# Kernel tuning notes

Measured on AMD Instinct MI355X. Metric: run time of the kernel, lower is better.

## Reference

```python
import jax, jax.numpy as jnp
import numpy as np

N, IN_DIM, OUT_DIM, HEADS = 3072, 512, 64, 8
EDGE_PROB = 0.01
NEG_SLOPE = 0.2


def setup_inputs() -> dict:
    key = jax.random.key(0)
    k1, k2, k3, k4, k5 = jax.random.split(key, 5)
    x = jax.random.normal(k1, (N, IN_DIM), dtype=jnp.float32)
    # sparse-ish dense adjacency mask with self-loops
    adj = (jax.random.uniform(k2, (N, N)) < EDGE_PROB).astype(jnp.float32)
    adj = jnp.maximum(adj, jnp.eye(N, dtype=jnp.float32))
    W = jax.random.normal(k3, (HEADS, IN_DIM, OUT_DIM), dtype=jnp.float32) * 0.1
    a_src = jax.random.normal(k4, (HEADS, OUT_DIM), dtype=jnp.float32) * 0.1
    a_dst = jax.random.normal(k5, (HEADS, OUT_DIM), dtype=jnp.float32) * 0.1
    return {"x": x, "adj": adj, "W": W, "a_src": a_src, "a_dst": a_dst}


def reference(x, adj, W, a_src, a_dst):
    # per-head linear projection: [H, N, OUT]
    h = jnp.einsum("ni,hio->hno", x, W)
    # attention logits e_ij = LeakyReLU(a_src . h_i + a_dst . h_j)
    f_src = jnp.einsum("hno,ho->hn", h, a_src)  # [H, N]
    f_dst = jnp.einsum("hno,ho->hn", h, a_dst)  # [H, N]
    e = f_src[:, :, None] + f_dst[:, None, :]   # [H, N, N]
    e = jax.nn.leaky_relu(e, negative_slope=NEG_SLOPE)
    # mask non-edges, row-softmax over neighbors
    e = jnp.where(adj[None] > 0, e, jnp.float32(-1e9))
    att = jax.nn.softmax(e, axis=-1)             # [H, N, N]
    # aggregate neighbor features per head
    out = jnp.einsum("hij,hjo->hio", att, h)     # [H, N, OUT]
    # concat heads along feature dim -> [N, H*OUT]
    return out.transpose(1, 0, 2).reshape(N, HEADS * OUT_DIM)
```

## Files before the change

### kernel.cpp

```cpp
#include <hip/hip_runtime.h>

#define N_NODES 3072
#define IN_DIM 512
#define OUT_DIM 64
#define HEADS 8
#define NEG_SLOPE 0.2f
#define MAX_E 128

typedef __attribute__((ext_vector_type(8))) short bf16x8;
typedef __attribute__((ext_vector_type(4))) float f32x4;

#define XFRAG_TILES (N_NODES / 16)
#define KTILES (IN_DIM / 32)
#define XFRAG_THREADS (XFRAG_TILES * KTILES * 64)
#define WFRAG_THREADS (HEADS * KTILES * 4 * 64)

__device__ inline unsigned short f2bf(float f) {
    union { float f; unsigned u; } v; v.f = f;
    unsigned r = (v.u + 0x7FFF + ((v.u >> 16) & 1)) >> 16;
    return (unsigned short)r;
}

__global__ __launch_bounds__(256) void gat_prep(
    const float* __restrict__ x, const float* __restrict__ W,
    short* __restrict__ xfrag, short* __restrict__ wfrag) {
    int tid = blockIdx.x * 256 + threadIdx.x;
    if (tid < XFRAG_THREADS) {
        int lane = tid & 63;
        int kt = (tid >> 6) & (KTILES - 1);
        int rt = tid >> 10;
        int m = rt * 16 + (lane & 15);
        int k0 = kt * 32 + (lane >> 4) * 8;
        const float4* xp = (const float4*)(x + (size_t)m * IN_DIM + k0);
        float4 v0 = xp[0], v1 = xp[1];
        bf16x8 r;
        r[0] = (short)f2bf(v0.x); r[1] = (short)f2bf(v0.y);
        r[2] = (short)f2bf(v0.z); r[3] = (short)f2bf(v0.w);
        r[4] = (short)f2bf(v1.x); r[5] = (short)f2bf(v1.y);
        r[6] = (short)f2bf(v1.z); r[7] = (short)f2bf(v1.w);
        ((bf16x8*)xfrag)[tid] = r;
    } else {
        int t2 = tid - XFRAG_THREADS;
        if (t2 >= WFRAG_THREADS) return;
        int lane = t2 & 63;
        int c = (t2 >> 6) & 3;
        int kt = (t2 >> 8) & (KTILES - 1);
        int head = t2 >> 12;
        int n = c * 16 + (lane & 15);
        int k0 = kt * 32 + (lane >> 4) * 8;
        const float* wp = W + ((size_t)head * IN_DIM + k0) * OUT_DIM + n;
        bf16x8 r;
#pragma unroll
        for (int j = 0; j < 8; ++j) r[j] = (short)f2bf(wp[(size_t)j * OUT_DIM]);
        ((bf16x8*)wfrag)[t2] = r;
    }
}

__global__ __launch_bounds__(256) void gat_proj(
    const short* __restrict__ xfrag, const short* __restrict__ wfrag,
    const float* __restrict__ a_src, const float* __restrict__ a_dst,
    unsigned short* __restrict__ hb, float* __restrict__ fsrc, float* __restrict__ fdst) {
    __shared__ float hs[32][OUT_DIM + 1];

    const int t = threadIdx.x;
    const int lane = t & 63;
    const int w = t >> 6;
    const int head = blockIdx.y;
    const int m0 = blockIdx.x * 32;
    const int rt0 = blockIdx.x * 2;

    const bf16x8* xa = (const bf16x8*)xfrag + (size_t)rt0 * 16 * 64 + lane;
    const bf16x8* wb = (const bf16x8*)wfrag + ((size_t)head * KTILES * 4 + w) * 64 + lane;

    f32x4 acc0 = {0.f, 0.f, 0.f, 0.f};
    f32x4 acc1 = {0.f, 0.f, 0.f, 0.f};
#pragma unroll
    for (int kt = 0; kt < KTILES; ++kt) {
        bf16x8 a0 = xa[kt * 64];
        bf16x8 a1 = xa[(16 + kt) * 64];
        bf16x8 b  = wb[kt * 4 * 64];
        acc0 = __builtin_amdgcn_mfma_f32_16x16x32_bf16(a0, b, acc0, 0, 0, 0);
        acc1 = __builtin_amdgcn_mfma_f32_16x16x32_bf16(a1, b, acc1, 0, 0, 0);
    }

    const int col = w * 16 + (lane & 15);
    const int r0 = (lane >> 4) * 4;
    unsigned short* hp = hb + (size_t)m0 * (HEADS * OUT_DIM) + head * OUT_DIM + col;
#pragma unroll
    for (int i2 = 0; i2 < 4; ++i2) {
        hs[r0 + i2][col] = acc0[i2];
        hs[r0 + 16 + i2][col] = acc1[i2];
        hp[(size_t)(r0 + i2) * (HEADS * OUT_DIM)] = f2bf(acc0[i2]);
        hp[(size_t)(r0 + 16 + i2) * (HEADS * OUT_DIM)] = f2bf(acc1[i2]);
    }
    __syncthreads();

    {
        const float* av = (t < 128 ? a_src : a_dst) + head * OUT_DIM;
        const int tt = t & 127;
        const int row = tt >> 2, part = tt & 3;
        float s = 0.f;
#pragma unroll
        for (int n = 0; n < 16; ++n) s += hs[row][part * 16 + n] * av[part * 16 + n];
        s += __shfl_xor(s, 1, 64);
        s += __shfl_xor(s, 2, 64);
        if (part == 0) {
            float* dst = (t < 128 ? fsrc : fdst);
            dst[head * N_NODES + m0 + row] = s;
        }
    }
}

__global__ __launch_bounds__(256) void gat_agg(
    const float* __restrict__ adj, const unsigned short* __restrict__ hb,
    const float* __restrict__ fsrc, const float* __restrict__ fdst,
    float* __restrict__ out) {
    __shared__ int s_idx[MAX_E];
    __shared__ float s_p[HEADS][MAX_E];
    __shared__ int s_cnt;

    const int i = blockIdx.x;
    const int t = threadIdx.x;
    if (t == 0) s_cnt = 0;
    __syncthreads();

    const float4* arow4 = (const float4*)(adj + (size_t)i * N_NODES);
#pragma unroll
    for (int it = 0; it < 3; ++it) {
        const int jj = t + it * 256;
        float4 v = arow4[jj];
        const int j = jj * 4;
        if (v.x > 0.f) { int s = atomicAdd(&s_cnt, 1); if (s < MAX_E) s_idx[s] = j; }
        if (v.y > 0.f) { int s = atomicAdd(&s_cnt, 1); if (s < MAX_E) s_idx[s] = j + 1; }
        if (v.z > 0.f) { int s = atomicAdd(&s_cnt, 1); if (s < MAX_E) s_idx[s] = j + 2; }
        if (v.w > 0.f) { int s = atomicAdd(&s_cnt, 1); if (s < MAX_E) s_idx[s] = j + 3; }
    }
    __syncthreads();
    const int E = min(s_cnt, MAX_E);

    const int w = t >> 6;
    const int lane = t & 63;
    const int half = lane >> 5;
    const int sl = lane & 31;
    const int head = 2 * w + half;

    const float fi = fsrc[head * N_NODES + i];

    float m = -1e30f;
    for (int k = sl; k < E; k += 32) {
        float e = fi + fdst[head * N_NODES + s_idx[k]];
        e = e > 0.f ? e : NEG_SLOPE * e;
        s_p[head][k] = e;
        m = fmaxf(m, e);
    }
#pragma unroll
    for (int o = 16; o; o >>= 1) m = fmaxf(m, __shfl_xor(m, o, 64));

    float sum = 0.f;
    for (int k = sl; k < E; k += 32) {
        float p = __expf(s_p[head][k] - m);
        s_p[head][k] = p;
        sum += p;
    }
#pragma unroll
    for (int o = 16; o; o >>= 1) sum += __shfl_xor(sum, o, 64);
    const float inv = 1.f / sum;

    __syncthreads();

    const unsigned short* hbase = hb + head * OUT_DIM + sl * 2;
    float a0 = 0.f, a1 = 0.f;
#pragma unroll 8
    for (int k = 0; k < E; ++k) {
        const int j = s_idx[k];
        const float p = s_p[head][k];
        const unsigned u = *(const unsigned*)(hbase + (size_t)j * (HEADS * OUT_DIM));
        a0 = fmaf(p, __uint_as_float(u << 16), a0);
        a1 = fmaf(p, __uint_as_float(u & 0xffff0000u), a1);
    }
    float2 r = {a0 * inv, a1 * inv};
    *(float2*)(out + (size_t)i * (HEADS * OUT_DIM) + head * OUT_DIM + sl * 2) = r;
}

extern "C" void kernel_launch(void* const* d_in, const int* in_sizes, int n_in,
                              void* d_out, int out_size, void* d_ws, size_t ws_size,
                              hipStream_t stream) {
    const float* x     = (const float*)d_in[0];
    const float* adj   = (const float*)d_in[1];
    const float* W     = (const float*)d_in[2];
    const float* a_src = (const float*)d_in[3];
    const float* a_dst = (const float*)d_in[4];
    float* out = (float*)d_out;

    float* fsrc = (float*)d_ws;
    float* fdst = fsrc + HEADS * N_NODES;
    unsigned short* hb = (unsigned short*)(fdst + HEADS * N_NODES);
    short* xfrag = (short*)(hb + (size_t)N_NODES * HEADS * OUT_DIM);
    short* wfrag = xfrag + (size_t)XFRAG_TILES * KTILES * 64 * 8;

    gat_prep<<<(XFRAG_THREADS + WFRAG_THREADS) / 256, 256, 0, stream>>>(
        x, W, xfrag, wfrag);
    gat_proj<<<dim3(N_NODES / 32, HEADS), 256, 0, stream>>>(
        xfrag, wfrag, a_src, a_dst, hb, fsrc, fdst);
    gat_agg<<<N_NODES, 256, 0, stream>>>(adj, hb, fsrc, fdst, out);
}
```

Before: 108.2 us.

## Move adjacency scan into prep kernel so it overlaps bf16 conversion

The adjacency-row scan that builds each node's neighbor list moves out of the aggregation kernel and into the prep kernel, which now runs extra blocks alongside the x/W bf16 fragment conversion. Neighbor indices and counts go to workspace, and the aggregation kernel reads them instead of streaming the 36 MB dense adjacency matrix. The aim is to run the bandwidth-heavy adjacency read in parallel with independent prep work and to shorten the critical aggregation kernel. It costs an extra global write and read of the compact edge lists, plus more workspace.

```diff
diff --git a/kernel.cpp b/kernel.cpp
--- a/kernel.cpp
+++ b/kernel.cpp
@@ -14,6 +14,7 @@
 #define KTILES (IN_DIM / 32)
 #define XFRAG_THREADS (XFRAG_TILES * KTILES * 64)
 #define WFRAG_THREADS (HEADS * KTILES * 4 * 64)
+#define PREP_BLOCKS ((XFRAG_THREADS + WFRAG_THREADS) / 256)
 
 __device__ inline unsigned short f2bf(float f) {
     union { float f; unsigned u; } v; v.f = f;
@@ -21,38 +22,69 @@
     return (unsigned short)r;
 }
 
-__global__ __launch_bounds__(256) void gat_prep(
+__global__ __launch_bounds__(256) void gat_prep_scan(
     const float* __restrict__ x, const float* __restrict__ W,
-    short* __restrict__ xfrag, short* __restrict__ wfrag) {
-    int tid = blockIdx.x * 256 + threadIdx.x;
-    if (tid < XFRAG_THREADS) {
-        int lane = tid & 63;
-        int kt = (tid >> 6) & (KTILES - 1);
-        int rt = tid >> 10;
-        int m = rt * 16 + (lane & 15);
-        int k0 = kt * 32 + (lane >> 4) * 8;
-        const float4* xp = (const float4*)(x + (size_t)m * IN_DIM + k0);
-        float4 v0 = xp[0], v1 = xp[1];
-        bf16x8 r;
-        r[0] = (short)f2bf(v0.x); r[1] = (short)f2bf(v0.y);
-        r[2] = (short)f2bf(v0.z); r[3] = (short)f2bf(v0.w);
-        r[4] = (short)f2bf(v1.x); r[5] = (short)f2bf(v1.y);
-        r[6] = (short)f2bf(v1.z); r[7] = (short)f2bf(v1.w);
-        ((bf16x8*)xfrag)[tid] = r;
+    const float* __restrict__ adj,
+    short* __restrict__ xfrag, short* __restrict__ wfrag,
+    int* __restrict__ e_idx, int* __restrict__ e_cnt) {
+    __shared__ int s_idx[MAX_E];
+    __shared__ int s_cnt;
+
+    const int b = blockIdx.x;
+    const int t = threadIdx.x;
+
+    if (b < N_NODES) {
+        const int i = b;
+        if (t == 0) s_cnt = 0;
+        __syncthreads();
+
+        const float4* arow4 = (const float4*)(adj + (size_t)i * N_NODES);
+#pragma unroll
+        for (int it = 0; it < 3; ++it) {
+            const int jj = t + it * 256;
+            float4 v = arow4[jj];
+            const int j = jj * 4;
+            if (v.x > 0.f) { int s = atomicAdd(&s_cnt, 1); if (s < MAX_E) s_idx[s] = j; }
+            if (v.y > 0.f) { int s = atomicAdd(&s_cnt, 1); if (s < MAX_E) s_idx[s] = j + 1; }
+            if (v.z > 0.f) { int s = atomicAdd(&s_cnt, 1); if (s < MAX_E) s_idx[s] = j + 2; }
+            if (v.w > 0.f) { int s = atomicAdd(&s_cnt, 1); if (s < MAX_E) s_idx[s] = j + 3; }
+        }
+        __syncthreads();
+        const int E = min(s_cnt, MAX_E);
+        if (t < E) e_idx[(size_t)i * MAX_E + t] = s_idx[t];
+        if (t == 0) e_cnt[i] = E;
     } else {
-        int t2 = tid - XFRAG_THREADS;
-        if (t2 >= WFRAG_THREADS) return;
-        int lane = t2 & 63;
-        int c = (t2 >> 6) & 3;
-        int kt = (t2 >> 8) & (KTILES - 1);
-        int head = t2 >> 12;
-        int n = c * 16 + (lane & 15);
-        int k0 = kt * 32 + (lane >> 4) * 8;
-        const float* wp = W + ((size_t)head * IN_DIM + k0) * OUT_DIM + n;
-        bf16x8 r;
-#pragma unroll
-        for (int j = 0; j < 8; ++j) r[j] = (short)f2bf(wp[(size_t)j * OUT_DIM]);
-        ((bf16x8*)wfrag)[t2] = r;
+        const int tid = (b - N_NODES) * 256 + t;
+        if (tid < XFRAG_THREADS) {
+            int lane = tid & 63;
+            int kt = (tid >> 6) & (KTILES - 1);
+            int rt = tid >> 10;
+            int m = rt * 16 + (lane & 15);
+            int k0 = kt * 32 + (lane >> 4) * 8;
+            const float4* xp = (const float4*)(x + (size_t)m * IN_DIM + k0);
+            float4 v0 = xp[0], v1 = xp[1];
+            bf16x8 r;
+            r[0] = (short)f2bf(v0.x); r[1] = (short)f2bf(v0.y);
+            r[2] = (short)f2bf(v0.z); r[3] = (short)f2bf(v0.w);
+            r[4] = (short)f2bf(v1.x); r[5] = (short)f2bf(v1.y);
+            r[6] = (short)f2bf(v1.z); r[7] = (short)f2bf(v1.w);
+            ((bf16x8*)xfrag)[tid] = r;
+        } else {
+            int t2 = tid - XFRAG_THREADS;
+            if (t2 < WFRAG_THREADS) {
+                int lane = t2 & 63;
+                int c = (t2 >> 6) & 3;
+                int kt = (t2 >> 8) & (KTILES - 1);
+                int head = t2 >> 12;
+                int n = c * 16 + (lane & 15);
+                int k0 = kt * 32 + (lane >> 4) * 8;
+                const float* wp = W + ((size_t)head * IN_DIM + k0) * OUT_DIM + n;
+                bf16x8 r;
+#pragma unroll
+                for (int j = 0; j < 8; ++j) r[j] = (short)f2bf(wp[(size_t)j * OUT_DIM]);
+                ((bf16x8*)wfrag)[t2] = r;
+            }
+        }
     }
 }
 
@@ -112,31 +144,18 @@
 }
 
 __global__ __launch_bounds__(256) void gat_agg(
-    const float* __restrict__ adj, const unsigned short* __restrict__ hb,
+    const int* __restrict__ e_idx, const int* __restrict__ e_cnt,
+    const unsigned short* __restrict__ hb,
     const float* __restrict__ fsrc, const float* __restrict__ fdst,
     float* __restrict__ out) {
     __shared__ int s_idx[MAX_E];
     __shared__ float s_p[HEADS][MAX_E];
-    __shared__ int s_cnt;
 
     const int i = blockIdx.x;
     const int t = threadIdx.x;
-    if (t == 0) s_cnt = 0;
+    const int E = e_cnt[i];
+    if (t < E) s_idx[t] = e_idx[(size_t)i * MAX_E + t];
     __syncthreads();
-
-    const float4* arow4 = (const float4*)(adj + (size_t)i * N_NODES);
-#pragma unroll
-    for (int it = 0; it < 3; ++it) {
-        const int jj = t + it * 256;
-        float4 v = arow4[jj];
-        const int j = jj * 4;
-        if (v.x > 0.f) { int s = atomicAdd(&s_cnt, 1); if (s < MAX_E) s_idx[s] = j; }
-        if (v.y > 0.f) { int s = atomicAdd(&s_cnt, 1); if (s < MAX_E) s_idx[s] = j + 1; }
-        if (v.z > 0.f) { int s = atomicAdd(&s_cnt, 1); if (s < MAX_E) s_idx[s] = j + 2; }
-        if (v.w > 0.f) { int s = atomicAdd(&s_cnt, 1); if (s < MAX_E) s_idx[s] = j + 3; }
-    }
-    __syncthreads();
-    const int E = min(s_cnt, MAX_E);
 
     const int w = t >> 6;
     const int lane = t & 63;
@@ -197,10 +216,12 @@
     unsigned short* hb = (unsigned short*)(fdst + HEADS * N_NODES);
     short* xfrag = (short*)(hb + (size_t)N_NODES * HEADS * OUT_DIM);
     short* wfrag = xfrag + (size_t)XFRAG_TILES * KTILES * 64 * 8;
-
-    gat_prep<<<(XFRAG_THREADS + WFRAG_THREADS) / 256, 256, 0, stream>>>(
-        x, W, xfrag, wfrag);
+    int* e_idx = (int*)(wfrag + (size_t)HEADS * KTILES * 4 * 64 * 8);
+    int* e_cnt = e_idx + (size_t)N_NODES * MAX_E;
+
+    gat_prep_scan<<<N_NODES + PREP_BLOCKS, 256, 0, stream>>>(
+        x, W, adj, xfrag, wfrag, e_idx, e_cnt);
     gat_proj<<<dim3(N_NODES / 32, HEADS), 256, 0, stream>>>(
         xfrag, wfrag, a_src, a_dst, hb, fsrc, fdst);
-    gat_agg<<<N_NODES, 256, 0, stream>>>(adj, hb, fsrc, fdst, out);
-}
+    gat_agg<<<N_NODES, 256, 0, stream>>>(e_idx, e_cnt, hb, fsrc, fdst, out);
+}
```

Measured after the change: 109.7 us. No clear change (+1.3%).
